# Performance work log

Measured on AMD Instinct MI355X. Metric: run time of the kernel, lower is better.

## Reference

```python
import jax, jax.numpy as jnp
from jax import lax
import numpy as np

B, N, C = 8, 10647, 80          # batch, total anchors (416px YOLOv3), COCO classes
MAX_BOXES = 100                  # yolo_max_boxes (per class and total, like combined NMS)
IOU_TH = 0.5
SCORE_TH = 0.3


def setup_inputs() -> dict:
    key = jax.random.key(0)
    k1, k2, k3, k4 = jax.random.split(key, 4)
    # valid corner-format boxes (x1,y1,x2,y2) in [0,1]
    xy = jax.random.uniform(k1, (B, N, 2), dtype=jnp.float32) * 0.9
    wh = jax.random.uniform(k2, (B, N, 2), dtype=jnp.float32) * 0.1 + 0.01
    boxes = jnp.concatenate([xy, xy + wh], axis=-1)
    confidence = jax.random.uniform(k3, (B, N, 1), dtype=jnp.float32)
    class_probs = jax.random.uniform(k4, (B, N, C), dtype=jnp.float32)
    return {"boxes": boxes, "confidence": confidence, "class_probs": class_probs}


def _iou_one_vs_all(box, boxes):
    # box [4], boxes [N,4], corner format
    x1 = jnp.maximum(box[0], boxes[:, 0])
    y1 = jnp.maximum(box[1], boxes[:, 1])
    x2 = jnp.minimum(box[2], boxes[:, 2])
    y2 = jnp.minimum(box[3], boxes[:, 3])
    inter = jnp.maximum(x2 - x1, 0.0) * jnp.maximum(y2 - y1, 0.0)
    area_a = (box[2] - box[0]) * (box[3] - box[1])
    area_b = (boxes[:, 2] - boxes[:, 0]) * (boxes[:, 3] - boxes[:, 1])
    return inter / (area_a + area_b - inter + 1e-9)


def _nms_one_class(scores_c, bxs):
    # scores_c [N], bxs [N,4]: greedy NMS, returns MAX_BOXES candidates
    s0 = jnp.where(scores_c > SCORE_TH, scores_c, -1.0)

    def step(cur, _):
        i = jnp.argmax(cur)
        sc = cur[i]
        b = bxs[i]
        ious = _iou_one_vs_all(b, bxs)
        nxt = jnp.where(ious > IOU_TH, -1.0, cur).at[i].set(-1.0)
        valid = sc > 0.0
        return nxt, (jnp.where(valid, sc, 0.0),
                     jnp.where(valid, b, jnp.zeros(4, b.dtype)),
                     valid)

    _, (ss, bb, vv) = lax.scan(step, s0, None, length=MAX_BOXES)
    return bb, ss, vv  # [M,4], [M], [M]


def reference(boxes, confidence, class_probs):
    # scores per class: objectness * class prob  -> [B, C, N]
    scores = jnp.transpose(confidence * class_probs, (0, 2, 1))
    per_class = jax.vmap(jax.vmap(_nms_one_class, in_axes=(0, None)), in_axes=(0, 0))
    cb, cs, cv = per_class(scores, boxes)           # [B,C,M,4], [B,C,M], [B,C,M]

    flat_s = cs.reshape(B, -1)                       # [B, C*M]
    flat_b = cb.reshape(B, -1, 4)
    flat_v = cv.reshape(B, -1)
    cls_ids = jnp.broadcast_to(
        jnp.arange(C, dtype=jnp.float32)[:, None], (C, MAX_BOXES)).reshape(-1)

    top_s, top_i = lax.top_k(flat_s, MAX_BOXES)      # merge across classes
    sel_b = jnp.take_along_axis(flat_b, top_i[..., None], axis=1)
    sel_v = jnp.take_along_axis(flat_v, top_i, axis=1)
    sel_c = jnp.where(sel_v, cls_ids[top_i], 0.0)
    sel_s = jnp.where(sel_v, top_s, 0.0)
    num_valid = jnp.sum(sel_v, axis=1).astype(jnp.int32)
    return sel_b, sel_s, sel_c, num_valid
```

## Files before the change

### kernel.cpp

```cpp
#include <hip/hip_runtime.h>

#define Bn 8
#define Nn 10647
#define Cn 80
#define MAXB 100
#define SCORE_TH 0.3f
#define BGUESS 0.82f
#define IOU_THR 0.5f
#define NBIN 4096
#define NB2 1024
#define SORT_CAP 256
#define TARGET 160
#define CH 128
#define PCAP 16
#define TOT (Cn * MAXB)
#define TOTQ (TOT / 4)
#define MREG 8

__device__ __forceinline__ int score_bin(float s) {
    int v = (int)(__float_as_uint(s) >> 12) - 0x3E999 + 1;
    v = v < 1 ? 1 : v;
    return v > NBIN - 1 ? NBIN - 1 : v;
}
__device__ __forceinline__ int score_bin2(float s) {
    int v = (int)(__float_as_uint(s) >> 14) - 0xFA66 + 1;
    v = v < 1 ? 1 : v;
    return v > NB2 - 1 ? NB2 - 1 : v;
}

__device__ __forceinline__ bool iou_gt(const float4 s, const float4 c) {
    float x1 = fmaxf(s.x, c.x), y1 = fmaxf(s.y, c.y);
    float x2 = fminf(s.z, c.z), y2 = fminf(s.w, c.w);
    float inter = fmaxf(x2 - x1, 0.0f) * fmaxf(y2 - y1, 0.0f);
    float aS = (s.z - s.x) * (s.w - s.y);
    float aC = (c.z - c.x) * (c.w - c.y);
    return inter > IOU_THR * (aS + aC - inter + 1e-9f);
}

__global__ __launch_bounds__(256) void collect(
    const float* __restrict__ conf, const float* __restrict__ cp,
    int* __restrict__ pcnt, unsigned long long* __restrict__ glist)
{
    __shared__ float lconf[88];
    __shared__ int cnt3[Cn];
    __shared__ int cnt9[Cn];
    int tid = threadIdx.x;
    int b = blockIdx.x / CH;
    int ch = blockIdx.x % CH;

    for (int i = tid; i < Cn; i += 256) { cnt3[i] = 0; cnt9[i] = 0; }

    const int totq = Nn * 20;
    const int per = (totq + CH - 1) / CH;
    int q0 = ch * per;
    int q1 = q0 + per; if (q1 > totq) q1 = totq;
    int n0 = q0 / 20;
    int nspan = (q1 - 1) / 20 - n0 + 1;

    const float* confB = conf + b * Nn;
    for (int i = tid; i < nspan; i += 256) lconf[i] = confB[n0 + i];
    __syncthreads();

    const float4* cp4 = (const float4*)(cp + (size_t)b * Nn * Cn);

    for (int q = q0 + tid; q < q1; q += 256) {
        float4 v = cp4[q];
        int n = q / 20;
        int c0 = (q % 20) * 4;
        float cf = lconf[n - n0];
        float sv[4] = {v.x, v.y, v.z, v.w};
#pragma unroll
        for (int e = 0; e < 4; ++e) {
            float s = cf * sv[e];
            if (s > SCORE_TH) {
                atomicAdd(&cnt3[c0 + e], 1);
                if (s > BGUESS) {
                    int pos = atomicAdd(&cnt9[c0 + e], 1);
                    if (pos < PCAP)
                        glist[((size_t)(b * Cn + c0 + e) * CH + ch) * PCAP + pos] =
                            ((unsigned long long)__float_as_uint(s) << 32) |
                            (unsigned)(Nn - 1 - n);
                }
            }
        }
    }
    __syncthreads();
    for (int c = tid; c < Cn; c += 256)
        pcnt[(size_t)(b * Cn + c) * CH + ch] = (cnt3[c] & 0xFFFF) | (cnt9[c] << 16);
}

__global__ __launch_bounds__(512) void nms_class(
    const float4* __restrict__ boxes, const float* __restrict__ conf,
    const float* __restrict__ cp,
    const int* __restrict__ pcnt, const unsigned long long* __restrict__ gkey,
    float* __restrict__ wss, float4* __restrict__ wsb)
{
    __shared__ unsigned long long keys[SORT_CAP];
    __shared__ float ssc[SORT_CAP];
    __shared__ float4 sbx[SORT_CAP];
    __shared__ float4 bxu[SORT_CAP];
    __shared__ unsigned short cj[SORT_CAP][3];
    __shared__ int ncA[SORT_CAP];
    __shared__ unsigned char selv[SORT_CAP], resv[SORT_CAP], confl[SORT_CAP];
    __shared__ int rpart[SORT_CAP];
    __shared__ int chc[CH], chOff[CH];
    __shared__ int hist2[NB2];
    __shared__ int suf[257];
    __shared__ int wtot[4];
    __shared__ int sh_cnt, sh_tot, sh_ovf, sh_hard, sh_B, sh_M, sh_nsel;

    int tid = threadIdx.x;
    int lane = tid & 63, wv = tid >> 6;
    int bc = blockIdx.x;
    int b = bc / Cn, c = bc % Cn;

    if (tid == 0) { sh_hard = 0; sh_nsel = 0; }
    for (int i = tid; i < SORT_CAP; i += 512) ncA[i] = 0;
    float* ws_s = wss + bc * MAXB;
    float4* ws_b = wsb + bc * MAXB;
    for (int i = tid; i < MAXB; i += 512) ws_s[i] = 0.0f;

    if (tid < 64) {
        const int* pC = pcnt + (size_t)(b * Cn + c) * CH;
        int pA = pC[lane];
        int pB = pC[64 + lane];
        int cA = pA >> 16, cB = pB >> 16;
        bool ovf = (cA > PCAP) || (cB > PCAP);
        cA = cA > PCAP ? PCAP : cA;
        cB = cB > PCAP ? PCAP : cB;
        chc[lane] = cA; chc[64 + lane] = cB;
        int iA = cA, iB = cB;
#pragma unroll
        for (int off = 1; off < 64; off <<= 1) {
            int oA = __shfl_up(iA, off);
            int oB = __shfl_up(iB, off);
            if (lane >= off) { iA += oA; iB += oB; }
        }
        int totA = __shfl(iA, 63);
        int cntAll = totA + __shfl(iB, 63);
        chOff[lane] = iA - cA;
        chOff[64 + lane] = totA + iB - cB;
        int t3 = (pA & 0xFFFF) + (pB & 0xFFFF);
#pragma unroll
        for (int off = 32; off > 0; off >>= 1) t3 += __shfl_down(t3, off);
        unsigned long long om = __ballot(ovf);
        if (lane == 0) { sh_cnt = cntAll; sh_tot = t3; sh_ovf = om ? 1 : 0; }
    }
    __syncthreads();

    int cnt = sh_cnt;
    int tot = sh_tot;
    bool fast = (!sh_ovf) && (cnt <= SORT_CAP);
    int M = fast ? cnt : 0;

    const float4* boxesB = boxes + (size_t)b * Nn;

    if (fast) {
        const unsigned long long* slotC = gkey + (size_t)(b * Cn + c) * CH * PCAP;
        for (int i = tid; i < CH * PCAP; i += 512) {
            int ch = i >> 4, j = i & (PCAP - 1);
            if (j < chc[ch]) keys[chOff[ch] + j] = slotC[i];
        }
    }
    __syncthreads();

    int cand = tid & 255, half = tid >> 8;
    bool act = (cand < M);

    unsigned long long k0 = 0;
    float4 b0 = make_float4(0, 0, 0, 0);
    if (act) k0 = keys[cand];
    if (act && half == 0) b0 = boxesB[Nn - 1 - (int)(k0 & 0xffffffffu)];
    int r0 = 0;
    if (act) {
#pragma unroll 4
        for (int j = half; j < M; j += 2) r0 += (keys[j] > k0) ? 1 : 0;
    }
    if (act && half == 1) rpart[cand] = r0;
    __syncthreads();
    if (act && half == 0) {
        int rank = r0 + rpart[cand];
        ssc[rank] = __uint_as_float((unsigned)(k0 >> 32));
        sbx[rank] = b0;
    }
    __syncthreads();

    if (act) {
        float4 tb = sbx[cand];
#pragma unroll 4
        for (int j = half; j < cand; j += 2) {
            float4 bj = sbx[j];
            if (iou_gt(bj, tb)) {
                int s = atomicAdd(&ncA[cand], 1);
                if (s < 3) cj[cand][s] = (unsigned short)j;
            }
        }
    }
    __syncthreads();
    if (tid < SORT_CAP && tid < M && ncA[tid] > 3) atomicOr(&sh_hard, 1);
    __syncthreads();

    if (!sh_hard) {
        bool mysel = false, myres = false;
        if (tid < SORT_CAP) {
            myres = (tid < M) ? (ncA[tid] == 0) : true;
            mysel = (tid < M) && myres;
            selv[tid] = mysel ? 1 : 0;
            resv[tid] = myres ? 1 : 0;
        }
        __syncthreads();
        while (true) {
            bool upd = false, upd_sel = false;
            if (tid < SORT_CAP && tid < M && !myres) {
                int nc = ncA[tid];
                bool allr = true, anysel = false;
                for (int k = 0; k < nc; ++k) {
                    int j = cj[tid][k];
                    allr = allr && (resv[j] != 0);
                    anysel = anysel || (selv[j] != 0);
                }
                if (allr) { upd = true; upd_sel = !anysel; }
            }
            __syncthreads();
            if (upd) {
                myres = true; mysel = upd_sel;
                selv[tid] = mysel ? 1 : 0; resv[tid] = 1;
            }
            int unres = __syncthreads_count((tid < SORT_CAP && tid < M && !myres) ? 1 : 0);
            if (unres == 0) break;
        }
        int v = (tid < SORT_CAP && mysel) ? 1 : 0;
        int incl = v;
        if (tid < SORT_CAP) {
#pragma unroll
            for (int off = 1; off < 64; off <<= 1) {
                int o = __shfl_up(incl, off);
                if (lane >= off) incl += o;
            }
            if (lane == 63) wtot[wv] = incl;
        }
        __syncthreads();
        if (tid < SORT_CAP) {
            int base = 0;
            for (int w = 0; w < wv; ++w) base += wtot[w];
            int pos = base + incl - v;
            if (v && pos < MAXB) { ws_s[pos] = ssc[tid]; ws_b[pos] = sbx[tid]; }
            if (tid == 0) sh_nsel = wtot[0] + wtot[1] + wtot[2] + wtot[3];
        }
        __syncthreads();
    } else {
        if (tid < SORT_CAP) confl[tid] = (tid < M && ncA[tid] > 0) ? 1 : 0;
        __syncthreads();
        if (tid < 64) {
            float4 sA = make_float4(0, 0, 0, 0), sB = make_float4(0, 0, 0, 0);
            int nsel = 0;
            for (int w0 = 0; w0 < M && nsel < MAXB; w0 += 64) {
                int wlim = M - w0; if (wlim > 64) wlim = 64;
                bool cfl = (tid < wlim) ? (confl[w0 + tid] != 0) : false;
                unsigned long long cmask = __ballot(cfl);
                int pos = 0;
                while (pos < wlim && nsel < MAXB) {
                    if (!((cmask >> pos) & 1ULL)) {
                        unsigned long long rest = cmask >> pos;
                        int run = rest ? (__ffsll(rest) - 1) : (wlim - pos);
                        if (run > wlim - pos) run = wlim - pos;
                        int avail = MAXB - nsel; if (run > avail) run = avail;
                        int d = (tid - (nsel & 63)) & 63;
                        if (d < run) {
                            int s = nsel + d;
                            int ci = w0 + pos + d;
                            float4 bx = sbx[ci];
                            if (s < 64) sA = bx; else sB = bx;
                            ws_s[s] = ssc[ci]; ws_b[s] = bx;
                        }
                        nsel += run; pos += run;
                    } else {
                        int ci = w0 + pos;
                        float4 bx = sbx[ci];
                        bool sup = (tid < nsel) && iou_gt(sA, bx);
                        if (tid + 64 < nsel) sup = sup || iou_gt(sB, bx);
                        if (__ballot(sup) == 0ULL) {
                            if (tid == (nsel & 63)) { if (nsel < 64) sA = bx; else sB = bx; }
                            if (tid == 0) { ws_s[nsel] = ssc[ci]; ws_b[nsel] = bx; }
                            ++nsel;
                        }
                        ++pos;
                    }
                }
            }
            if (tid == 0) sh_nsel = nsel;
        }
        __syncthreads();
    }

    bool needSlow = (!fast) || !((sh_nsel >= MAXB) || (cnt == tot));
    if (!needSlow) return;

    for (int i = tid; i < MAXB; i += 512) ws_s[i] = 0.0f;
    for (int i = tid; i < NB2; i += 512) hist2[i] = 0;
    if (tid == 0) sh_nsel = 0;
    __syncthreads();

    const float* confB = conf + b * Nn;
    const float* cpB = cp + (size_t)b * Nn * Cn + c;
    for (int n = tid; n < Nn; n += 512) {
        float s = confB[n] * cpB[(size_t)n * Cn];
        if (s > SCORE_TH) atomicAdd(&hist2[score_bin2(s)], 1);
    }
    __syncthreads();

    float4 sA = make_float4(0, 0, 0, 0), sB = make_float4(0, 0, 0, 0);
    int hi = NB2;
    int round = 0;

    while (true) {
        if (tid < 256) {
            int ps = 0;
#pragma unroll
            for (int u = 0; u < 4; ++u) ps += hist2[tid * 4 + u];
            int p = ps;
#pragma unroll
            for (int off = 1; off < 64; off <<= 1) {
                int v = __shfl_down(p, off);
                if (lane + off < 64) p += v;
            }
            if (lane == 0) wtot[wv] = p;
            suf[tid] = p;
        }
        __syncthreads();
        if (tid < 256) {
            int add = 0;
            for (int w2 = wv + 1; w2 < 4; ++w2) add += wtot[w2];
            suf[tid] = suf[tid] + add;
            if (tid == 0) suf[256] = 0;
        }
        __syncthreads();

        int total = suf[0];
        if (total == 0) break;

        int target = total < TARGET ? total : TARGET;
        if (tid < 256 && suf[tid] >= target && suf[tid + 1] < target) sh_B = tid;
        if (tid == 0) sh_M = 0;
        __syncthreads();
        if (tid == 0) {
            int g = sh_B;
            int running = suf[g + 1];
            int B = g * 4;
            for (int u = 3; u >= 0; --u) {
                running += hist2[g * 4 + u];
                if (running >= target) { B = g * 4 + u; break; }
            }
            sh_B = B;
        }
        __syncthreads();
        int B = sh_B;

        for (int n = tid; n < Nn; n += 512) {
            float s = confB[n] * cpB[(size_t)n * Cn];
            if (s > SCORE_TH) {
                int bin = score_bin2(s);
                if (bin >= B && bin < hi) {
                    int pos2 = atomicAdd(&sh_M, 1);
                    if (pos2 < SORT_CAP)
                        keys[pos2] = ((unsigned long long)__float_as_uint(s) << 32) |
                                     (unsigned)(Nn - 1 - n);
                }
            }
        }
        __syncthreads();
        int M2 = sh_M; if (M2 > SORT_CAP) M2 = SORT_CAP;

        unsigned long long mk = 0;
        float4 mb = make_float4(0, 0, 0, 0);
        if (tid < 256) {
            if (tid < M2) { mk = keys[tid]; mb = boxesB[Nn - 1 - (int)(mk & 0xffffffffu)]; }
            bxu[tid] = mb;
        }
        __syncthreads();

        if (tid < 256) {
            int rank = 0;
            bool cfl = (round > 0);
            for (int j = 0; j < M2; ++j) {
                unsigned long long kk = keys[j];
                float4 bj = bxu[j];
                bool gt = kk > mk;
                rank += gt ? 1 : 0;
                if (round == 0) cfl = cfl || (gt && iou_gt(bj, mb));
            }
            if (tid < M2) {
                ssc[rank] = __uint_as_float((unsigned)(mk >> 32));
                sbx[rank] = mb; confl[rank] = cfl ? 1 : 0;
            }
        }
        __syncthreads();

        if (tid < 64) {
            int nsel = sh_nsel;
            for (int w0 = 0; w0 < M2 && nsel < MAXB; w0 += 64) {
                int wlim = M2 - w0; if (wlim > 64) wlim = 64;
                bool cfl2 = (tid < wlim) ? (confl[w0 + tid] != 0) : false;
                unsigned long long cmask = __ballot(cfl2);
                int pos = 0;
                while (pos < wlim && nsel < MAXB) {
                    if (!((cmask >> pos) & 1ULL)) {
                        unsigned long long rest = cmask >> pos;
                        int run = rest ? (__ffsll(rest) - 1) : (wlim - pos);
                        if (run > wlim - pos) run = wlim - pos;
                        int avail = MAXB - nsel; if (run > avail) run = avail;
                        int d = (tid - (nsel & 63)) & 63;
                        if (d < run) {
                            int s = nsel + d;
                            int ci = w0 + pos + d;
                            float4 bx = sbx[ci];
                            if (s < 64) sA = bx; else sB = bx;
                            ws_s[s] = ssc[ci]; ws_b[s] = bx;
                        }
                        nsel += run; pos += run;
                    } else {
                        int ci = w0 + pos;
                        float4 bx = sbx[ci];
                        bool sup = (tid < nsel) && iou_gt(sA, bx);
                        if (tid + 64 < nsel) sup = sup || iou_gt(sB, bx);
                        if (__ballot(sup) == 0ULL) {
                            if (tid == (nsel & 63)) { if (nsel < 64) sA = bx; else sB = bx; }
                            if (tid == 0) { ws_s[nsel] = ssc[ci]; ws_b[nsel] = bx; }
                            ++nsel;
                        }
                        ++pos;
                    }
                }
            }
            if (tid == 0) sh_nsel = nsel;
        }
        __syncthreads();
        if (sh_nsel >= MAXB) break;
        for (int i = B + tid; i < NB2; i += 512) hist2[i] = 0;
        hi = B;
        ++round;
        __syncthreads();
    }
}

__global__ __launch_bounds__(256) void merge_topk(
    const float* __restrict__ wss, const float4* __restrict__ wsb,
    float* __restrict__ out)
{
    __shared__ int hist[NBIN];
    __shared__ int suf[257];
    __shared__ int wtot[4];
    __shared__ unsigned long long keys[SORT_CAP];
    __shared__ unsigned long long skeys[SORT_CAP];
    __shared__ int sh_B, sh_M;

    int tid = threadIdx.x, b = blockIdx.x;
    int lane = tid & 63, wv = tid >> 6;
    for (int i = tid; i < NBIN / 4; i += 256) ((int4*)hist)[i] = make_int4(0, 0, 0, 0);
    if (tid == 0) sh_M = 0;
    skeys[tid] = 0ULL;
    __syncthreads();

    const float4* w4 = (const float4*)(wss + b * TOT);
    float4 rr[MREG];
#pragma unroll
    for (int k = 0; k < MREG; ++k) {
        int q = tid + k * 256;
        rr[k] = (q < TOTQ) ? w4[q] : make_float4(0, 0, 0, 0);
    }
#pragma unroll
    for (int k = 0; k < MREG; ++k) {
        float4 v = rr[k];
        if (v.x > 0.0f) atomicAdd(&hist[score_bin(v.x)], 1);
        if (v.y > 0.0f) atomicAdd(&hist[score_bin(v.y)], 1);
        if (v.z > 0.0f) atomicAdd(&hist[score_bin(v.z)], 1);
        if (v.w > 0.0f) atomicAdd(&hist[score_bin(v.w)], 1);
    }
    __syncthreads();

    int ps = 0;
#pragma unroll
    for (int u = 0; u < 16; ++u) ps += hist[tid * 16 + u];
    int p = ps;
#pragma unroll
    for (int off = 1; off < 64; off <<= 1) {
        int v = __shfl_down(p, off);
        if (lane + off < 64) p += v;
    }
    if (lane == 0) wtot[wv] = p;
    __syncthreads();
    int add = 0;
    for (int w2 = wv + 1; w2 < 4; ++w2) add += wtot[w2];
    suf[tid] = p + add;
    if (tid == 0) suf[256] = 0;
    __syncthreads();

    int total = suf[0];
    int target = total < MAXB ? total : MAXB;

    if (total > 0) {
        if (suf[tid] >= target && suf[tid + 1] < target) sh_B = tid;
    }
    __syncthreads();
    if (total > 0 && tid == 0) {
        int g = sh_B;
        int running = suf[g + 1];
        int B = g * 16;
        for (int u = 15; u >= 0; --u) {
            running += hist[g * 16 + u];
            if (running >= target) { B = g * 16 + u; break; }
        }
        sh_B = B;
    }
    __syncthreads();
    if (total > 0) {
        int B = sh_B;
#pragma unroll
        for (int k = 0; k < MREG; ++k) {
            int q = tid + k * 256;
            if (q < TOTQ) {
                float4 v = rr[k];
                int ib = q * 4;
                float sv[4] = {v.x, v.y, v.z, v.w};
#pragma unroll
                for (int e = 0; e < 4; ++e) {
                    float s = sv[e];
                    if (s > 0.0f && score_bin(s) >= B) {
                        int pos = atomicAdd(&sh_M, 1);
                        if (pos < SORT_CAP)
                            keys[pos] = ((unsigned long long)__float_as_uint(s) << 32) |
                                        (unsigned)(TOT - 1 - (ib + e));
                    }
                }
            }
        }
    }
    __syncthreads();
    int M = sh_M; if (M > SORT_CAP) M = SORT_CAP;

    unsigned long long mykey = (tid < M) ? keys[tid] : 0ULL;
    int rank = 0;
    for (int j = 0; j < M; ++j) rank += (keys[j] > mykey) ? 1 : 0;
    if (tid < M) skeys[rank] = mykey;
    __syncthreads();

    bool valid = false;
    if (tid < MAXB) {
        unsigned long long g = skeys[tid];
        valid = (g != 0ULL);
        float s = valid ? __uint_as_float((unsigned)(g >> 32)) : 0.0f;
        int f = TOT - 1 - (int)(g & 0xffffffffu);
        float4 bx = make_float4(0, 0, 0, 0);
        float cls = 0.0f;
        if (valid) { bx = wsb[b * TOT + f]; cls = (float)(f / MAXB); }
        ((float4*)out)[b * MAXB + tid] = bx;
        out[Bn * MAXB * 4 + b * MAXB + tid] = s;
        out[Bn * MAXB * 5 + b * MAXB + tid] = cls;
    }
    int nv = __syncthreads_count(valid);
    if (tid == 0) out[Bn * MAXB * 6 + b] = (float)nv;
}

extern "C" void kernel_launch(void* const* d_in, const int* in_sizes, int n_in,
                              void* d_out, int out_size, void* d_ws, size_t ws_size,
                              hipStream_t stream) {
    const float4* boxes = (const float4*)d_in[0];
    const float* conf   = (const float*)d_in[1];
    const float* cp     = (const float*)d_in[2];
    float* out = (float*)d_out;

    char* ws = (char*)d_ws;
    int* pcnt = (int*)(ws + 0);
    unsigned long long* gkey = (unsigned long long*)(ws + 327680);
    float* wss = (float*)(ws + 10813440);
    float4* wsb = (float4*)(ws + 11069440);

    collect<<<Bn * CH, 256, 0, stream>>>(conf, cp, pcnt, gkey);
    nms_class<<<Bn * Cn, 512, 0, stream>>>(boxes, conf, cp, pcnt, gkey, wss, wsb);
    merge_topk<<<Bn, 256, 0, stream>>>(wss, wsb, out);
}
```

Baseline: 48.40 us.

## Fuse cross-class merge into NMS kernel via last-block-done counter

Removes the separate merge_topk launch. The last per-class NMS block of each batch, detected with an atomic done counter and threadfences, now runs the top-100 merge itself, using the coarser 1024-bin histogram. The collect kernel also stops counting exact above-threshold scores per chunk and records only a per-chunk flag for scores below the guess threshold. The slow-path check becomes 'any such score exists', which replaces the count equality test. This saves a kernel launch and some shared atomics, but the tail merge now runs in a single block after the others finish and needs extra fences.

```diff
diff --git a/kernel.cpp b/kernel.cpp
--- a/kernel.cpp
+++ b/kernel.cpp
@@ -7,7 +7,6 @@
 #define SCORE_TH 0.3f
 #define BGUESS 0.82f
 #define IOU_THR 0.5f
-#define NBIN 4096
 #define NB2 1024
 #define SORT_CAP 256
 #define TARGET 160
@@ -15,13 +14,7 @@
 #define PCAP 16
 #define TOT (Cn * MAXB)
 #define TOTQ (TOT / 4)
-#define MREG 8
-
-__device__ __forceinline__ int score_bin(float s) {
-    int v = (int)(__float_as_uint(s) >> 12) - 0x3E999 + 1;
-    v = v < 1 ? 1 : v;
-    return v > NBIN - 1 ? NBIN - 1 : v;
-}
+
 __device__ __forceinline__ int score_bin2(float s) {
     int v = (int)(__float_as_uint(s) >> 14) - 0xFA66 + 1;
     v = v < 1 ? 1 : v;
@@ -39,16 +32,18 @@
 
 __global__ __launch_bounds__(256) void collect(
     const float* __restrict__ conf, const float* __restrict__ cp,
-    int* __restrict__ pcnt, unsigned long long* __restrict__ glist)
+    int* __restrict__ pcnt, unsigned long long* __restrict__ glist,
+    int* __restrict__ done)
 {
     __shared__ float lconf[88];
-    __shared__ int cnt3[Cn];
     __shared__ int cnt9[Cn];
+    __shared__ unsigned char lflag[Cn];
     int tid = threadIdx.x;
     int b = blockIdx.x / CH;
     int ch = blockIdx.x % CH;
 
-    for (int i = tid; i < Cn; i += 256) { cnt3[i] = 0; cnt9[i] = 0; }
+    if (blockIdx.x == 0 && tid < Bn) done[tid] = 0;
+    for (int i = tid; i < Cn; i += 256) { cnt9[i] = 0; lflag[i] = 0; }
 
     const int totq = Nn * 20;
     const int per = (totq + CH - 1) / CH;
@@ -72,30 +67,31 @@
 #pragma unroll
         for (int e = 0; e < 4; ++e) {
             float s = cf * sv[e];
-            if (s > SCORE_TH) {
-                atomicAdd(&cnt3[c0 + e], 1);
-                if (s > BGUESS) {
-                    int pos = atomicAdd(&cnt9[c0 + e], 1);
-                    if (pos < PCAP)
-                        glist[((size_t)(b * Cn + c0 + e) * CH + ch) * PCAP + pos] =
-                            ((unsigned long long)__float_as_uint(s) << 32) |
-                            (unsigned)(Nn - 1 - n);
-                }
+            if (s > BGUESS) {
+                int pos = atomicAdd(&cnt9[c0 + e], 1);
+                if (pos < PCAP)
+                    glist[((size_t)(b * Cn + c0 + e) * CH + ch) * PCAP + pos] =
+                        ((unsigned long long)__float_as_uint(s) << 32) |
+                        (unsigned)(Nn - 1 - n);
+            } else if (s > SCORE_TH) {
+                lflag[c0 + e] = 1;
             }
         }
     }
     __syncthreads();
     for (int c = tid; c < Cn; c += 256)
-        pcnt[(size_t)(b * Cn + c) * CH + ch] = (cnt3[c] & 0xFFFF) | (cnt9[c] << 16);
+        pcnt[(size_t)(b * Cn + c) * CH + ch] = (int)lflag[c] | (cnt9[c] << 16);
 }
 
 __global__ __launch_bounds__(512) void nms_class(
     const float4* __restrict__ boxes, const float* __restrict__ conf,
     const float* __restrict__ cp,
     const int* __restrict__ pcnt, const unsigned long long* __restrict__ gkey,
-    float* __restrict__ wss, float4* __restrict__ wsb)
+    float* __restrict__ wss, float4* __restrict__ wsb,
+    float* __restrict__ out, int* __restrict__ done)
 {
     __shared__ unsigned long long keys[SORT_CAP];
+    __shared__ unsigned long long skeys[SORT_CAP];
     __shared__ float ssc[SORT_CAP];
     __shared__ float4 sbx[SORT_CAP];
     __shared__ float4 bxu[SORT_CAP];
@@ -107,7 +103,7 @@
     __shared__ int hist2[NB2];
     __shared__ int suf[257];
     __shared__ int wtot[4];
-    __shared__ int sh_cnt, sh_tot, sh_ovf, sh_hard, sh_B, sh_M, sh_nsel;
+    __shared__ int sh_cnt, sh_any, sh_ovf, sh_hard, sh_B, sh_M, sh_nsel;
 
     int tid = threadIdx.x;
     int lane = tid & 63, wv = tid >> 6;
@@ -140,16 +136,18 @@
         int cntAll = totA + __shfl(iB, 63);
         chOff[lane] = iA - cA;
         chOff[64 + lane] = totA + iB - cB;
-        int t3 = (pA & 0xFFFF) + (pB & 0xFFFF);
-#pragma unroll
-        for (int off = 32; off > 0; off >>= 1) t3 += __shfl_down(t3, off);
+        bool anyUn = (((pA | pB) & 0xFFFF) != 0);
+        unsigned long long am = __ballot(anyUn);
         unsigned long long om = __ballot(ovf);
-        if (lane == 0) { sh_cnt = cntAll; sh_tot = t3; sh_ovf = om ? 1 : 0; }
+        if (lane == 0) {
+            sh_cnt = cntAll;
+            sh_any = am ? 1 : 0;
+            sh_ovf = om ? 1 : 0;
+        }
     }
     __syncthreads();
 
     int cnt = sh_cnt;
-    int tot = sh_tot;
     bool fast = (!sh_ovf) && (cnt <= SORT_CAP);
     int M = fast ? cnt : 0;
 
@@ -293,239 +291,239 @@
         __syncthreads();
     }
 
-    bool needSlow = (!fast) || !((sh_nsel >= MAXB) || (cnt == tot));
-    if (!needSlow) return;
-
-    for (int i = tid; i < MAXB; i += 512) ws_s[i] = 0.0f;
-    for (int i = tid; i < NB2; i += 512) hist2[i] = 0;
-    if (tid == 0) sh_nsel = 0;
-    __syncthreads();
-
-    const float* confB = conf + b * Nn;
-    const float* cpB = cp + (size_t)b * Nn * Cn + c;
-    for (int n = tid; n < Nn; n += 512) {
-        float s = confB[n] * cpB[(size_t)n * Cn];
-        if (s > SCORE_TH) atomicAdd(&hist2[score_bin2(s)], 1);
-    }
-    __syncthreads();
-
-    float4 sA = make_float4(0, 0, 0, 0), sB = make_float4(0, 0, 0, 0);
-    int hi = NB2;
-    int round = 0;
-
-    while (true) {
-        if (tid < 256) {
-            int ps = 0;
-#pragma unroll
-            for (int u = 0; u < 4; ++u) ps += hist2[tid * 4 + u];
-            int p = ps;
-#pragma unroll
-            for (int off = 1; off < 64; off <<= 1) {
-                int v = __shfl_down(p, off);
-                if (lane + off < 64) p += v;
-            }
-            if (lane == 0) wtot[wv] = p;
-            suf[tid] = p;
-        }
-        __syncthreads();
-        if (tid < 256) {
-            int add = 0;
-            for (int w2 = wv + 1; w2 < 4; ++w2) add += wtot[w2];
-            suf[tid] = suf[tid] + add;
-            if (tid == 0) suf[256] = 0;
-        }
-        __syncthreads();
-
-        int total = suf[0];
-        if (total == 0) break;
-
-        int target = total < TARGET ? total : TARGET;
-        if (tid < 256 && suf[tid] >= target && suf[tid + 1] < target) sh_B = tid;
-        if (tid == 0) sh_M = 0;
-        __syncthreads();
-        if (tid == 0) {
-            int g = sh_B;
-            int running = suf[g + 1];
-            int B = g * 4;
-            for (int u = 3; u >= 0; --u) {
-                running += hist2[g * 4 + u];
-                if (running >= target) { B = g * 4 + u; break; }
-            }
-            sh_B = B;
-        }
-        __syncthreads();
-        int B = sh_B;
-
+    bool needSlow = (!fast) || (sh_nsel < MAXB && sh_any != 0);
+    if (needSlow) {
+        for (int i = tid; i < MAXB; i += 512) ws_s[i] = 0.0f;
+        for (int i = tid; i < NB2; i += 512) hist2[i] = 0;
+        if (tid == 0) sh_nsel = 0;
+        __syncthreads();
+
+        const float* confB = conf + b * Nn;
+        const float* cpB = cp + (size_t)b * Nn * Cn + c;
         for (int n = tid; n < Nn; n += 512) {
             float s = confB[n] * cpB[(size_t)n * Cn];
-            if (s > SCORE_TH) {
-                int bin = score_bin2(s);
-                if (bin >= B && bin < hi) {
-                    int pos2 = atomicAdd(&sh_M, 1);
-                    if (pos2 < SORT_CAP)
-                        keys[pos2] = ((unsigned long long)__float_as_uint(s) << 32) |
-                                     (unsigned)(Nn - 1 - n);
-                }
-            }
-        }
-        __syncthreads();
-        int M2 = sh_M; if (M2 > SORT_CAP) M2 = SORT_CAP;
-
-        unsigned long long mk = 0;
-        float4 mb = make_float4(0, 0, 0, 0);
-        if (tid < 256) {
-            if (tid < M2) { mk = keys[tid]; mb = boxesB[Nn - 1 - (int)(mk & 0xffffffffu)]; }
-            bxu[tid] = mb;
-        }
-        __syncthreads();
-
-        if (tid < 256) {
-            int rank = 0;
-            bool cfl = (round > 0);
-            for (int j = 0; j < M2; ++j) {
-                unsigned long long kk = keys[j];
-                float4 bj = bxu[j];
-                bool gt = kk > mk;
-                rank += gt ? 1 : 0;
-                if (round == 0) cfl = cfl || (gt && iou_gt(bj, mb));
-            }
-            if (tid < M2) {
-                ssc[rank] = __uint_as_float((unsigned)(mk >> 32));
-                sbx[rank] = mb; confl[rank] = cfl ? 1 : 0;
-            }
-        }
-        __syncthreads();
-
-        if (tid < 64) {
-            int nsel = sh_nsel;
-            for (int w0 = 0; w0 < M2 && nsel < MAXB; w0 += 64) {
-                int wlim = M2 - w0; if (wlim > 64) wlim = 64;
-                bool cfl2 = (tid < wlim) ? (confl[w0 + tid] != 0) : false;
-                unsigned long long cmask = __ballot(cfl2);
-                int pos = 0;
-                while (pos < wlim && nsel < MAXB) {
-                    if (!((cmask >> pos) & 1ULL)) {
-                        unsigned long long rest = cmask >> pos;
-                        int run = rest ? (__ffsll(rest) - 1) : (wlim - pos);
-                        if (run > wlim - pos) run = wlim - pos;
-                        int avail = MAXB - nsel; if (run > avail) run = avail;
-                        int d = (tid - (nsel & 63)) & 63;
-                        if (d < run) {
-                            int s = nsel + d;
-                            int ci = w0 + pos + d;
+            if (s > SCORE_TH) atomicAdd(&hist2[score_bin2(s)], 1);
+        }
+        __syncthreads();
+
+        float4 sA = make_float4(0, 0, 0, 0), sB = make_float4(0, 0, 0, 0);
+        int hi = NB2;
+        int round = 0;
+
+        while (true) {
+            if (tid < 256) {
+                int ps = 0;
+#pragma unroll
+                for (int u = 0; u < 4; ++u) ps += hist2[tid * 4 + u];
+                int p = ps;
+#pragma unroll
+                for (int off = 1; off < 64; off <<= 1) {
+                    int v = __shfl_down(p, off);
+                    if (lane + off < 64) p += v;
+                }
+                if (lane == 0) wtot[wv] = p;
+                suf[tid] = p;
+            }
+            __syncthreads();
+            if (tid < 256) {
+                int add = 0;
+                for (int w2 = wv + 1; w2 < 4; ++w2) add += wtot[w2];
+                suf[tid] = suf[tid] + add;
+                if (tid == 0) suf[256] = 0;
+            }
+            __syncthreads();
+
+            int total = suf[0];
+            if (total == 0) break;
+
+            int target = total < TARGET ? total : TARGET;
+            if (tid < 256 && suf[tid] >= target && suf[tid + 1] < target) sh_B = tid;
+            if (tid == 0) sh_M = 0;
+            __syncthreads();
+            if (tid == 0) {
+                int g = sh_B;
+                int running = suf[g + 1];
+                int B = g * 4;
+                for (int u = 3; u >= 0; --u) {
+                    running += hist2[g * 4 + u];
+                    if (running >= target) { B = g * 4 + u; break; }
+                }
+                sh_B = B;
+            }
+            __syncthreads();
+            int B = sh_B;
+
+            for (int n = tid; n < Nn; n += 512) {
+                float s = confB[n] * cpB[(size_t)n * Cn];
+                if (s > SCORE_TH) {
+                    int bin = score_bin2(s);
+                    if (bin >= B && bin < hi) {
+                        int pos2 = atomicAdd(&sh_M, 1);
+                        if (pos2 < SORT_CAP)
+                            keys[pos2] = ((unsigned long long)__float_as_uint(s) << 32) |
+                                         (unsigned)(Nn - 1 - n);
+                    }
+                }
+            }
+            __syncthreads();
+            int M2 = sh_M; if (M2 > SORT_CAP) M2 = SORT_CAP;
+
+            unsigned long long mk = 0;
+            float4 mb = make_float4(0, 0, 0, 0);
+            if (tid < 256) {
+                if (tid < M2) { mk = keys[tid]; mb = boxesB[Nn - 1 - (int)(mk & 0xffffffffu)]; }
+                bxu[tid] = mb;
+            }
+            __syncthreads();
+
+            if (tid < 256) {
+                int rank = 0;
+                bool cfl = (round > 0);
+                for (int j = 0; j < M2; ++j) {
+                    unsigned long long kk = keys[j];
+                    float4 bj = bxu[j];
+                    bool gt = kk > mk;
+                    rank += gt ? 1 : 0;
+                    if (round == 0) cfl = cfl || (gt && iou_gt(bj, mb));
+                }
+                if (tid < M2) {
+                    ssc[rank] = __uint_as_float((unsigned)(mk >> 32));
+                    sbx[rank] = mb; confl[rank] = cfl ? 1 : 0;
+                }
+            }
+            __syncthreads();
+
+            if (tid < 64) {
+                int nsel = sh_nsel;
+                for (int w0 = 0; w0 < M2 && nsel < MAXB; w0 += 64) {
+                    int wlim = M2 - w0; if (wlim > 64) wlim = 64;
+                    bool cfl2 = (tid < wlim) ? (confl[w0 + tid] != 0) : false;
+                    unsigned long long cmask = __ballot(cfl2);
+                    int pos = 0;
+                    while (pos < wlim && nsel < MAXB) {
+                        if (!((cmask >> pos) & 1ULL)) {
+                            unsigned long long rest = cmask >> pos;
+                            int run = rest ? (__ffsll(rest) - 1) : (wlim - pos);
+                            if (run > wlim - pos) run = wlim - pos;
+                            int avail = MAXB - nsel; if (run > avail) run = avail;
+                            int d = (tid - (nsel & 63)) & 63;
+                            if (d < run) {
+                                int s = nsel + d;
+                                int ci = w0 + pos + d;
+                                float4 bx = sbx[ci];
+                                if (s < 64) sA = bx; else sB = bx;
+                                ws_s[s] = ssc[ci]; ws_b[s] = bx;
+                            }
+                            nsel += run; pos += run;
+                        } else {
+                            int ci = w0 + pos;
                             float4 bx = sbx[ci];
-                            if (s < 64) sA = bx; else sB = bx;
-                            ws_s[s] = ssc[ci]; ws_b[s] = bx;
+                            bool sup = (tid < nsel) && iou_gt(sA, bx);
+                            if (tid + 64 < nsel) sup = sup || iou_gt(sB, bx);
+                            if (__ballot(sup) == 0ULL) {
+                                if (tid == (nsel & 63)) { if (nsel < 64) sA = bx; else sB = bx; }
+                                if (tid == 0) { ws_s[nsel] = ssc[ci]; ws_b[nsel] = bx; }
+                                ++nsel;
+                            }
+                            ++pos;
                         }
-                        nsel += run; pos += run;
-                    } else {
-                        int ci = w0 + pos;
-                        float4 bx = sbx[ci];
-                        bool sup = (tid < nsel) && iou_gt(sA, bx);
-                        if (tid + 64 < nsel) sup = sup || iou_gt(sB, bx);
-                        if (__ballot(sup) == 0ULL) {
-                            if (tid == (nsel & 63)) { if (nsel < 64) sA = bx; else sB = bx; }
-                            if (tid == 0) { ws_s[nsel] = ssc[ci]; ws_b[nsel] = bx; }
-                            ++nsel;
-                        }
-                        ++pos;
                     }
                 }
-            }
-            if (tid == 0) sh_nsel = nsel;
-        }
-        __syncthreads();
-        if (sh_nsel >= MAXB) break;
-        for (int i = B + tid; i < NB2; i += 512) hist2[i] = 0;
-        hi = B;
-        ++round;
-        __syncthreads();
-    }
-}
-
-__global__ __launch_bounds__(256) void merge_topk(
-    const float* __restrict__ wss, const float4* __restrict__ wsb,
-    float* __restrict__ out)
-{
-    __shared__ int hist[NBIN];
-    __shared__ int suf[257];
-    __shared__ int wtot[4];
-    __shared__ unsigned long long keys[SORT_CAP];
-    __shared__ unsigned long long skeys[SORT_CAP];
-    __shared__ int sh_B, sh_M;
-
-    int tid = threadIdx.x, b = blockIdx.x;
-    int lane = tid & 63, wv = tid >> 6;
-    for (int i = tid; i < NBIN / 4; i += 256) ((int4*)hist)[i] = make_int4(0, 0, 0, 0);
-    if (tid == 0) sh_M = 0;
-    skeys[tid] = 0ULL;
+                if (tid == 0) sh_nsel = nsel;
+            }
+            __syncthreads();
+            if (sh_nsel >= MAXB) break;
+            for (int i = B + tid; i < NB2; i += 512) hist2[i] = 0;
+            hi = B;
+            ++round;
+            __syncthreads();
+        }
+    }
+
+    __syncthreads();
+    if (tid == 0) {
+        __threadfence();
+        int old = atomicAdd(&done[b], 1);
+        sh_ovf = (old == Cn - 1) ? 1 : 0;
+    }
+    __syncthreads();
+    if (!sh_ovf) return;
+    __threadfence();
+
+    for (int i = tid; i < NB2; i += 512) hist2[i] = 0;
+    if (tid == 0) { sh_M = 0; sh_B = 0; }
+    if (tid < SORT_CAP) skeys[tid] = 0ULL;
     __syncthreads();
 
     const float4* w4 = (const float4*)(wss + b * TOT);
-    float4 rr[MREG];
-#pragma unroll
-    for (int k = 0; k < MREG; ++k) {
-        int q = tid + k * 256;
+    float4 rr[4];
+#pragma unroll
+    for (int k = 0; k < 4; ++k) {
+        int q = tid + k * 512;
         rr[k] = (q < TOTQ) ? w4[q] : make_float4(0, 0, 0, 0);
     }
 #pragma unroll
-    for (int k = 0; k < MREG; ++k) {
+    for (int k = 0; k < 4; ++k) {
         float4 v = rr[k];
-        if (v.x > 0.0f) atomicAdd(&hist[score_bin(v.x)], 1);
-        if (v.y > 0.0f) atomicAdd(&hist[score_bin(v.y)], 1);
-        if (v.z > 0.0f) atomicAdd(&hist[score_bin(v.z)], 1);
-        if (v.w > 0.0f) atomicAdd(&hist[score_bin(v.w)], 1);
-    }
-    __syncthreads();
-
-    int ps = 0;
-#pragma unroll
-    for (int u = 0; u < 16; ++u) ps += hist[tid * 16 + u];
-    int p = ps;
-#pragma unroll
-    for (int off = 1; off < 64; off <<= 1) {
-        int v = __shfl_down(p, off);
-        if (lane + off < 64) p += v;
-    }
-    if (lane == 0) wtot[wv] = p;
-    __syncthreads();
-    int add = 0;
-    for (int w2 = wv + 1; w2 < 4; ++w2) add += wtot[w2];
-    suf[tid] = p + add;
-    if (tid == 0) suf[256] = 0;
-    __syncthreads();
-
-    int total = suf[0];
-    int target = total < MAXB ? total : MAXB;
-
-    if (total > 0) {
-        if (suf[tid] >= target && suf[tid + 1] < target) sh_B = tid;
-    }
-    __syncthreads();
-    if (total > 0 && tid == 0) {
+        if (v.x > 0.0f) atomicAdd(&hist2[score_bin2(v.x)], 1);
+        if (v.y > 0.0f) atomicAdd(&hist2[score_bin2(v.y)], 1);
+        if (v.z > 0.0f) atomicAdd(&hist2[score_bin2(v.z)], 1);
+        if (v.w > 0.0f) atomicAdd(&hist2[score_bin2(v.w)], 1);
+    }
+    __syncthreads();
+
+    if (tid < 256) {
+        int ps = 0;
+#pragma unroll
+        for (int u = 0; u < 4; ++u) ps += hist2[tid * 4 + u];
+        int p = ps;
+#pragma unroll
+        for (int off = 1; off < 64; off <<= 1) {
+            int v = __shfl_down(p, off);
+            if (lane + off < 64) p += v;
+        }
+        if (lane == 0) wtot[wv] = p;
+        suf[tid] = p;
+    }
+    __syncthreads();
+    if (tid < 256) {
+        int add = 0;
+        for (int w2 = wv + 1; w2 < 4; ++w2) add += wtot[w2];
+        suf[tid] = suf[tid] + add;
+        if (tid == 0) suf[256] = 0;
+    }
+    __syncthreads();
+
+    int totalm = suf[0];
+    int target = totalm < MAXB ? totalm : MAXB;
+    if (totalm > 0) {
+        if (tid < 256 && suf[tid] >= target && suf[tid + 1] < target) sh_B = tid;
+    }
+    __syncthreads();
+    if (totalm > 0 && tid == 0) {
         int g = sh_B;
         int running = suf[g + 1];
-        int B = g * 16;
-        for (int u = 15; u >= 0; --u) {
-            running += hist[g * 16 + u];
-            if (running >= target) { B = g * 16 + u; break; }
+        int B = g * 4;
+        for (int u = 3; u >= 0; --u) {
+            running += hist2[g * 4 + u];
+            if (running >= target) { B = g * 4 + u; break; }
         }
         sh_B = B;
     }
     __syncthreads();
-    if (total > 0) {
+    if (totalm > 0) {
         int B = sh_B;
 #pragma unroll
-        for (int k = 0; k < MREG; ++k) {
-            int q = tid + k * 256;
+        for (int k = 0; k < 4; ++k) {
+            int q = tid + k * 512;
             if (q < TOTQ) {
                 float4 v = rr[k];
                 int ib = q * 4;
-                float sv[4] = {v.x, v.y, v.z, v.w};
+                float svv[4] = {v.x, v.y, v.z, v.w};
 #pragma unroll
                 for (int e = 0; e < 4; ++e) {
-                    float s = sv[e];
-                    if (s > 0.0f && score_bin(s) >= B) {
+                    float s = svv[e];
+                    if (s > 0.0f && score_bin2(s) >= B) {
                         int pos = atomicAdd(&sh_M, 1);
                         if (pos < SORT_CAP)
                             keys[pos] = ((unsigned long long)__float_as_uint(s) << 32) |
@@ -536,12 +534,14 @@
         }
     }
     __syncthreads();
-    int M = sh_M; if (M > SORT_CAP) M = SORT_CAP;
-
-    unsigned long long mykey = (tid < M) ? keys[tid] : 0ULL;
-    int rank = 0;
-    for (int j = 0; j < M; ++j) rank += (keys[j] > mykey) ? 1 : 0;
-    if (tid < M) skeys[rank] = mykey;
+    int Mm = sh_M; if (Mm > SORT_CAP) Mm = SORT_CAP;
+
+    if (tid < 256) {
+        unsigned long long mykey = (tid < Mm) ? keys[tid] : 0ULL;
+        int rank = 0;
+        for (int j = 0; j < Mm; ++j) rank += (keys[j] > mykey) ? 1 : 0;
+        if (tid < Mm) skeys[rank] = mykey;
+    }
     __syncthreads();
 
     bool valid = false;
@@ -574,8 +574,9 @@
     unsigned long long* gkey = (unsigned long long*)(ws + 327680);
     float* wss = (float*)(ws + 10813440);
     float4* wsb = (float4*)(ws + 11069440);
-
-    collect<<<Bn * CH, 256, 0, stream>>>(conf, cp, pcnt, gkey);
-    nms_class<<<Bn * Cn, 512, 0, stream>>>(boxes, conf, cp, pcnt, gkey, wss, wsb);
-    merge_topk<<<Bn, 256, 0, stream>>>(wss, wsb, out);
+    int* done = (int*)(ws + 12093440);
+
+    collect<<<Bn * CH, 256, 0, stream>>>(conf, cp, pcnt, gkey, done);
+    nms_class<<<Bn * Cn, 512, 0, stream>>>(boxes, conf, cp, pcnt, gkey,
+                                           wss, wsb, out, done);
 }
```

Result: slower. 55.51 us (+14.7%).
